# Performance work log

Hardware: AMD Instinct MI355X
Metric: run time of the kernel (lower is better)

Reference implementation:

```python
import jax, jax.numpy as jnp
import numpy as np

B, D, C_IN, C_OUT = 256, 8, 2, 4


def setup_inputs() -> dict:
    key = jax.random.key(0)
    k1, k2, k3, k4 = jax.random.split(key, 4)
    rho = jax.random.normal(k1, (B, C_IN * D * D, C_IN * D * D), dtype=jnp.float32)
    ux = jax.random.normal(k2, (D, D), dtype=jnp.float32)
    uy = jax.random.normal(k3, (D, D), dtype=jnp.float32)
    uc = jax.random.normal(k4, (C_OUT, C_OUT), dtype=jnp.float32)
    return {"rho": rho, "ux": ux, "uy": uy, "uc": uc}


def _insert_channels(rho, d, c_in, c_out):
    # Faithful port of _InsertChannels: move each (channel f, pixel i,j) row/col
    # index to channel f + (c_out - c_in) in the enlarged register.
    b = rho.shape[0]
    x = jnp.arange(c_in * d * d)
    f = x // (d * d)                       # channel index
    i = (x % (d * d)) // d                 # row pixel
    j = x % d                              # col pixel
    new_idx = i * d + j + (f + (c_out - c_in)) * d * d  # [c_in*d^2]
    big = jnp.zeros((b, c_out * d * d, c_out * d * d), dtype=rho.dtype)
    # Indices are a bijection onto a sub-block, so add == set (matches
    # index_put_(..., accumulate=True) in torch).
    return big.at[:, new_idx[:, None], new_idx[None, :]].add(rho)


def reference(rho, ux, uy, uc):
    d = ux.shape[0]
    c_out = uc.shape[0]
    c_in = rho.shape[1] // (d * d)
    # channel insertion (c_in < c_out path)
    rho_big = _insert_channels(rho, d, c_in, c_out)        # [b, C, C], C = c_out*d^2
    # u = kron(uc, kron(ux, uy))
    u = jnp.kron(uc, jnp.kron(ux, uy))                     # [C, C]
    # new_rho = u @ rho @ u^H (real float32 -> conj is identity, transpose only)
    u_rho = jnp.einsum('pq,bqr->bpr', u, rho_big)
    new_rho = jnp.einsum('bpr,sr->bps', u_rho, u)
    return new_rho
```

## Files before the change

### kernel.cpp

```cpp
#include <hip/hip_runtime.h>


#define TPB 512

typedef float nfloat4 __attribute__((ext_vector_type(4)));

__global__ __launch_bounds__(TPB, 2) void qconv_fused(
    const float* __restrict__ rho,
    const float* __restrict__ ux,
    const float* __restrict__ uy,
    const float* __restrict__ uc,
    float* __restrict__ out)
{
    __shared__ alignas(16) float L[4][64][68];

    const int tid  = threadIdx.x;
    const int bid  = blockIdx.x;
    const int b    = bid >> 1;
    const int h    = bid & 1;
    const int w    = tid >> 6;
    const int lane = tid & 63;
    const int pyp  = lane >> 3, qyp = lane & 7;

    const int qg  = tid & 15;
    const int csh = (tid >> 4) & 1;
    const int spl = tid >> 5;

    float e0[4], e1[4];
#pragma unroll
    for (int c = 0; c < 4; ++c) { e0[c] = uc[c*4+2]; e1[c] = uc[c*4+3]; }
    float* ob = out + (size_t)b * 65536;

    float X[64];

    if (w < 4) {
        const int c1 = w >> 1, c2 = w & 1;
        const int px = lane >> 3, qx = lane & 7;
        const float* rb = rho + (size_t)b * 16384
                        + (size_t)((c1 << 6) + (px << 3)) * 128 + (c2 << 6) + (qx << 3);

#pragma unroll
        for (int py = 0; py < 8; ++py) {
            float4 lo = *(const float4*)(rb + py * 128);
            float4 hi = *(const float4*)(rb + py * 128 + 4);
            X[py*8+0]=lo.x; X[py*8+1]=lo.y; X[py*8+2]=lo.z; X[py*8+3]=lo.w;
            X[py*8+4]=hi.x; X[py*8+5]=hi.y; X[py*8+6]=hi.z; X[py*8+7]=hi.w;
        }

#pragma unroll
        for (int r = 0; r < 8; ++r) {
            float t[8];
#pragma unroll
            for (int j = 0; j < 8; ++j) {
                float a = 0.f;
#pragma unroll
                for (int k = 0; k < 8; ++k) a += uy[j*8+k] * X[r*8+k];
                t[j] = a;
            }
#pragma unroll
            for (int j = 0; j < 8; ++j) X[r*8+j] = t[j];
        }

#pragma unroll
        for (int cc = 0; cc < 8; ++cc) {
            float t[8];
#pragma unroll
            for (int i = 0; i < 8; ++i) {
                float a = 0.f;
#pragma unroll
                for (int k = 0; k < 8; ++k) a += uy[i*8+k] * X[k*8+cc];
                t[i] = a;
            }
#pragma unroll
            for (int i = 0; i < 8; ++i) X[i*8+cc] = t[i];
        }

#pragma unroll
        for (int e = 0; e < 64; ++e)
            L[w][e][lane ^ (((e >> 3) & 7) << 2)] = X[e];
        __asm__ volatile("s_waitcnt lgkmcnt(0)" ::: "memory");
        {
            const int sw = ((lane >> 3) & 7) << 2;
#pragma unroll
            for (int f4 = 0; f4 < 16; ++f4) {
                float4 v = *(const float4*)&L[w][lane][(f4 * 4) ^ sw];
                X[f4*4+0]=v.x; X[f4*4+1]=v.y; X[f4*4+2]=v.z; X[f4*4+3]=v.w;
            }
        }

#pragma unroll
        for (int p = 0; p < 8; ++p) {
            float t[8];
#pragma unroll
            for (int j = 0; j < 8; ++j) {
                float a = 0.f;
#pragma unroll
                for (int k = 0; k < 8; ++k) a += ux[j*8+k] * X[p*8+k];
                t[j] = a;
            }
#pragma unroll
            for (int j = 0; j < 8; ++j) X[p*8+j] = t[j];
        }
    }

#pragma unroll
    for (int s2 = 0; s2 < 2; ++s2) {
        const int s = 2*h + s2;
        if (w < 4) {
#pragma unroll
            for (int i2 = 0; i2 < 2; ++i2) {
                const int i = 2*s + i2;
#pragma unroll
                for (int j = 0; j < 8; ++j) {
                    float acc = 0.f;
#pragma unroll
                    for (int k = 0; k < 8; ++k) acc += ux[i*8+k] * X[k*8+j];
                    L[w][i*8+pyp][j*8+qyp] = acc;
                }
            }
        }
        __asm__ volatile("s_waitcnt lgkmcnt(0)" ::: "memory");
        __builtin_amdgcn_s_barrier();
        __asm__ volatile("" ::: "memory");

        const int sp = 16*s + spl;
        float4 wv[4];
#pragma unroll
        for (int ww = 0; ww < 4; ++ww) wv[ww] = *(const float4*)&L[ww][sp][qg * 4];
#pragma unroll
        for (int c = 0; c < 4; ++c) {
#pragma unroll
            for (int cs2 = 0; cs2 < 2; ++cs2) {
                const int cs = 2*csh + cs2;
                const float k00 = e0[c]*e0[cs], k01 = e0[c]*e1[cs];
                const float k10 = e1[c]*e0[cs], k11 = e1[c]*e1[cs];
                nfloat4 v;
                v.x = k00*wv[0].x + k01*wv[1].x + k10*wv[2].x + k11*wv[3].x;
                v.y = k00*wv[0].y + k01*wv[1].y + k10*wv[2].y + k11*wv[3].y;
                v.z = k00*wv[0].z + k01*wv[1].z + k10*wv[2].z + k11*wv[3].z;
                v.w = k00*wv[0].w + k01*wv[1].w + k10*wv[2].w + k11*wv[3].w;
                __builtin_nontemporal_store(v,
                    (nfloat4*)&ob[(size_t)((c*64 + sp) * 256 + cs*64 + qg*4)]);
            }
        }
    }
}

extern "C" void kernel_launch(void* const* d_in, const int* in_sizes, int n_in,
                              void* d_out, int out_size, void* d_ws, size_t ws_size,
                              hipStream_t stream) {
    const float* rho = (const float*)d_in[0];
    const float* ux  = (const float*)d_in[1];
    const float* uy  = (const float*)d_in[2];
    const float* uc  = (const float*)d_in[3];
    float* out = (float*)d_out;
    qconv_fused<<<dim3(512), dim3(TPB), 0, stream>>>(rho, ux, uy, uc, out);
}
```

Before: 96.09 us.

## Split fused kernel into two stages through workspace for wider parallelism

Replaces the single fused kernel with two launches. The first runs a 64-thread block per (batch, quadrant) that applies the uy/ux transforms and writes the 64x64 intermediate to the workspace. The second uses many 256-thread blocks to apply the uc channel mix and write the output. The aim is to remove the idle waves and barriers of the fused design and spread the output writes over more blocks. The cost is an extra global write and read of a 16 MB intermediate and a second launch. The fused kernel stays as a fallback when the workspace is too small.

```diff
diff --git a/kernel.cpp b/kernel.cpp
--- a/kernel.cpp
+++ b/kernel.cpp
@@ -5,11 +5,144 @@
 
 typedef float nfloat4 __attribute__((ext_vector_type(4)));
 
-__global__ __launch_bounds__(TPB, 2) void qconv_fused(
+__global__ __launch_bounds__(64) void qconv_stage1(
     const float* __restrict__ rho,
     const float* __restrict__ ux,
     const float* __restrict__ uy,
+    float* __restrict__ ws)
+{
+    __shared__ alignas(16) float T[64][68];
+
+    const int lane = threadIdx.x;
+    const int b    = blockIdx.x & 255;
+    const int quad = blockIdx.x >> 8;
+    const int c1 = quad >> 1, c2 = quad & 1;
+    const int px = lane >> 3, qx = lane & 7;
+
+    const float* rb = rho + (size_t)b * 16384
+                    + (size_t)((c1 << 6) + (px << 3)) * 128 + (c2 << 6) + (qx << 3);
+
+    float X[64];
+#pragma unroll
+    for (int py = 0; py < 8; ++py) {
+        float4 lo = *(const float4*)(rb + py * 128);
+        float4 hi = *(const float4*)(rb + py * 128 + 4);
+        X[py*8+0]=lo.x; X[py*8+1]=lo.y; X[py*8+2]=lo.z; X[py*8+3]=lo.w;
+        X[py*8+4]=hi.x; X[py*8+5]=hi.y; X[py*8+6]=hi.z; X[py*8+7]=hi.w;
+    }
+
+#pragma unroll
+    for (int r = 0; r < 8; ++r) {
+        float t[8];
+#pragma unroll
+        for (int j = 0; j < 8; ++j) {
+            float a = 0.f;
+#pragma unroll
+            for (int k = 0; k < 8; ++k) a += uy[j*8+k] * X[r*8+k];
+            t[j] = a;
+        }
+#pragma unroll
+        for (int j = 0; j < 8; ++j) X[r*8+j] = t[j];
+    }
+
+#pragma unroll
+    for (int cc = 0; cc < 8; ++cc) {
+        float t[8];
+#pragma unroll
+        for (int i = 0; i < 8; ++i) {
+            float a = 0.f;
+#pragma unroll
+            for (int k = 0; k < 8; ++k) a += uy[i*8+k] * X[k*8+cc];
+            t[i] = a;
+        }
+#pragma unroll
+        for (int i = 0; i < 8; ++i) X[i*8+cc] = t[i];
+    }
+
+#pragma unroll
+    for (int e = 0; e < 64; ++e)
+        T[e][lane ^ (((e >> 3) & 7) << 2)] = X[e];
+    __asm__ volatile("s_waitcnt lgkmcnt(0)" ::: "memory");
+    {
+        const int sw = ((lane >> 3) & 7) << 2;
+#pragma unroll
+        for (int f4 = 0; f4 < 16; ++f4) {
+            float4 v = *(const float4*)&T[lane][(f4 * 4) ^ sw];
+            X[f4*4+0]=v.x; X[f4*4+1]=v.y; X[f4*4+2]=v.z; X[f4*4+3]=v.w;
+        }
+    }
+
+#pragma unroll
+    for (int p = 0; p < 8; ++p) {
+        float t[8];
+#pragma unroll
+        for (int j = 0; j < 8; ++j) {
+            float a = 0.f;
+#pragma unroll
+            for (int k = 0; k < 8; ++k) a += ux[j*8+k] * X[p*8+k];
+            t[j] = a;
+        }
+#pragma unroll
+        for (int j = 0; j < 8; ++j) X[p*8+j] = t[j];
+    }
+
+    float* wbase = ws + ((size_t)(b * 4 + quad) * 64) * 64 + lane;
+#pragma unroll
+    for (int i = 0; i < 8; ++i) {
+#pragma unroll
+        for (int j = 0; j < 8; ++j) {
+            float acc = 0.f;
+#pragma unroll
+            for (int k = 0; k < 8; ++k) acc += ux[i*8+k] * X[k*8+j];
+            wbase[(size_t)(i*8 + j) * 64] = acc;
+        }
+    }
+}
+
+__global__ __launch_bounds__(256, 8) void qconv_stage2(
+    const float* __restrict__ ws,
     const float* __restrict__ uc,
+    float* __restrict__ out)
+{
+    const int tid = threadIdx.x;
+    const int b   = blockIdx.x & 255;
+    const int z   = blockIdx.x >> 8;
+    const int q   = tid & 15;
+    const int csh = (tid >> 4) & 1;
+    const int p   = z * 8 + (tid >> 5);
+
+    float e0[4], e1[4];
+#pragma unroll
+    for (int c = 0; c < 4; ++c) { e0[c] = uc[c*4+2]; e1[c] = uc[c*4+3]; }
+
+    const float* wb = ws + (size_t)b * 16384
+                    + (size_t)(((p >> 3) * 8 + (q >> 1)) * 64 + (p & 7) * 8 + (q & 1) * 4);
+    nfloat4 wv[4];
+#pragma unroll
+    for (int quad = 0; quad < 4; ++quad)
+        wv[quad] = *(const nfloat4*)(wb + quad * 4096);
+
+    float* ob = out + (size_t)b * 65536 + (size_t)p * 256 + q * 4;
+#pragma unroll
+    for (int c = 0; c < 4; ++c) {
+#pragma unroll
+        for (int cs2 = 0; cs2 < 2; ++cs2) {
+            const int cs = 2 * csh + cs2;
+            const float k00 = e0[c]*e0[cs], k01 = e0[c]*e1[cs];
+            const float k10 = e1[c]*e0[cs], k11 = e1[c]*e1[cs];
+            nfloat4 v;
+            v.x = k00*wv[0].x + k01*wv[1].x + k10*wv[2].x + k11*wv[3].x;
+            v.y = k00*wv[0].y + k01*wv[1].y + k10*wv[2].y + k11*wv[3].y;
+            v.z = k00*wv[0].z + k01*wv[1].z + k10*wv[2].z + k11*wv[3].z;
+            v.w = k00*wv[0].w + k01*wv[1].w + k10*wv[2].w + k11*wv[3].w;
+            __builtin_nontemporal_store(v, (nfloat4*)(ob + c * 16384 + cs * 64));
+        }
+    }
+}
+
+__global__ __launch_bounds__(TPB, 2) void qconv_fused(
+    const float* __restrict__ rho, const float* __restrict__ ux,
+    const float* __restrict__ uy, const float* __restrict__ uc,
     float* __restrict__ out)
 {
     __shared__ alignas(16) float L[4][64][68];
@@ -38,7 +171,6 @@
         const int px = lane >> 3, qx = lane & 7;
         const float* rb = rho + (size_t)b * 16384
                         + (size_t)((c1 << 6) + (px << 3)) * 128 + (c2 << 6) + (qx << 3);
-
 #pragma unroll
         for (int py = 0; py < 8; ++py) {
             float4 lo = *(const float4*)(rb + py * 128);
@@ -46,7 +178,6 @@
             X[py*8+0]=lo.x; X[py*8+1]=lo.y; X[py*8+2]=lo.z; X[py*8+3]=lo.w;
             X[py*8+4]=hi.x; X[py*8+5]=hi.y; X[py*8+6]=hi.z; X[py*8+7]=hi.w;
         }
-
 #pragma unroll
         for (int r = 0; r < 8; ++r) {
             float t[8];
@@ -60,7 +191,6 @@
 #pragma unroll
             for (int j = 0; j < 8; ++j) X[r*8+j] = t[j];
         }
-
 #pragma unroll
         for (int cc = 0; cc < 8; ++cc) {
             float t[8];
@@ -74,7 +204,6 @@
 #pragma unroll
             for (int i = 0; i < 8; ++i) X[i*8+cc] = t[i];
         }
-
 #pragma unroll
         for (int e = 0; e < 64; ++e)
             L[w][e][lane ^ (((e >> 3) & 7) << 2)] = X[e];
@@ -87,7 +216,6 @@
                 X[f4*4+0]=v.x; X[f4*4+1]=v.y; X[f4*4+2]=v.z; X[f4*4+3]=v.w;
             }
         }
-
 #pragma unroll
         for (int p = 0; p < 8; ++p) {
             float t[8];
@@ -154,5 +282,13 @@
     const float* uy  = (const float*)d_in[2];
     const float* uc  = (const float*)d_in[3];
     float* out = (float*)d_out;
-    qconv_fused<<<dim3(512), dim3(TPB), 0, stream>>>(rho, ux, uy, uc, out);
-}
+
+    const size_t ws_needed = (size_t)256 * 4 * 64 * 64 * sizeof(float);
+    if (ws_size >= ws_needed && d_ws != nullptr) {
+        float* ws = (float*)d_ws;
+        qconv_stage1<<<dim3(1024), dim3(64),  0, stream>>>(rho, ux, uy, ws);
+        qconv_stage2<<<dim3(2048), dim3(256), 0, stream>>>(ws, uc, out);
+    } else {
+        qconv_fused<<<dim3(512), dim3(TPB), 0, stream>>>(rho, ux, uy, uc, out);
+    }
+}
```

After: 98.34 us. 1.02x slower.
